# Kernel tuning notes

Hardware: AMD Instinct MI355X
Metric: run time of the kernel (lower is better)

## Reference

```python
import jax, jax.numpy as jnp
import numpy as np

TAU = 0.5  # init tau
EPS = 1e-8  # F.cosine_similarity eps


def setup_inputs() -> dict:
    key = jax.random.key(0)
    k1, k2 = jax.random.split(key)
    N, D, NUM_CLASSES = 4096, 1024, 128
    layer_embeds = jax.random.normal(k1, (N, D), dtype=jnp.float32)
    y_true = jax.random.randint(k2, (N,), 0, NUM_CLASSES, dtype=jnp.int64)
    return {"layer_embeds": layer_embeds, "y_true": y_true}


def reference(layer_embeds, y_true):
    N = layer_embeds.shape[0]
    # batched cosine similarity, scaled like the original: (cos + 1) * 0.5 * tau
    norms = jnp.maximum(jnp.linalg.norm(layer_embeds, axis=1), EPS)  # [N]
    cos = (layer_embeds @ layer_embeds.T) / (norms[:, None] * norms[None, :])  # [N, N]
    S = (cos + 1.0) * 0.5 * TAU

    same = y_true[:, None] == y_true[None, :]  # [N, N]
    eye = jnp.eye(N, dtype=bool)
    pos_mask = same & ~eye            # same-label pairs, j != i
    neg_mask = ~same                  # different-label pairs (diag excluded since same there)

    # column 0: first positive (in j order), else stays 0
    has_pos = pos_mask.any(axis=1)
    first_pos = jnp.argmax(pos_mask, axis=1)
    pos_val = jnp.where(has_pos, S[jnp.arange(N), first_pos], 0.0)  # [N]

    # negatives fill columns 1.. in j order: col = 1 + (#negatives with j' < j)
    negi = neg_mask.astype(jnp.int32)
    col = 1 + jnp.cumsum(negi, axis=1) - negi  # [N, N]
    W = 2 * N  # pad one dummy column for non-negative entries
    cols = jnp.where(neg_mask, col, W - 1)
    rows = jnp.broadcast_to(jnp.arange(N)[:, None], (N, N))
    loss_temp = jnp.zeros((N, W), dtype=jnp.float32)
    loss_temp = loss_temp.at[rows, cols].set(jnp.where(neg_mask, S, 0.0))
    loss_temp = loss_temp.at[:, 0].set(pos_val)
    loss_temp = loss_temp[:, : 2 * N - 1]  # [N, 2N-1], matches torch buffer

    # -log_softmax, take column 0, sum over rows, divide by N
    lse = jax.nn.logsumexp(loss_temp, axis=1)  # [N]
    loss = jnp.sum(lse - loss_temp[:, 0]) / N
    return loss
```

## Files before the change

### kernel.cpp

```cpp
#include <hip/hip_runtime.h>
#include <hip/hip_bf16.h>
#include <math.h>

#define NN 4096
#define DD 1024
#define NCLS 128
#define TAU 0.5f
#define EPSV 1e-8f
#define NB_GEMM 528

typedef __bf16 bf16;
typedef __bf16 bf16x8 __attribute__((ext_vector_type(8)));
typedef __bf16 bf16x4 __attribute__((ext_vector_type(4)));
typedef float f32x4 __attribute__((ext_vector_type(4)));

__device__ __forceinline__ void gl2lds16(const void* g, void* l) {
    __builtin_amdgcn_global_load_lds(
        (const __attribute__((address_space(1))) void*)g,
        (__attribute__((address_space(3))) void*)l,
        16, 0, 0);
}

__global__ __launch_bounds__(256) void k_prep(const float* __restrict__ X,
                                              const int* __restrict__ y,
                                              bf16* __restrict__ Xn,
                                              float* __restrict__ rsum,
                                              float* __restrict__ posv,
                                              int* __restrict__ cnt,
                                              int* __restrict__ fpos) {
    const int t = threadIdx.x;
    if (blockIdx.x == 0) {
        __shared__ int sc[NCLS], s1[NCLS], s2[NCLS];
        if (t < NCLS) { sc[t] = 0; s1[t] = 0x7fffffff; s2[t] = 0x7fffffff; }
        __syncthreads();
        int yv[16];
#pragma unroll
        for (int k = 0; k < 16; ++k) {
            int i = t + k * 256;
            yv[k] = y[i];
            atomicAdd(&sc[yv[k]], 1);
            atomicMin(&s1[yv[k]], i);
        }
        __syncthreads();
#pragma unroll
        for (int k = 0; k < 16; ++k) {
            int i = t + k * 256;
            if (s1[yv[k]] != i) atomicMin(&s2[yv[k]], i);
        }
        __syncthreads();
#pragma unroll
        for (int k = 0; k < 16; ++k) {
            int i = t + k * 256;
            int c = yv[k];
            fpos[i] = (sc[c] >= 2) ? (s1[c] == i ? s2[c] : s1[c]) : -1;
        }
        if (t < NCLS) cnt[t] = sc[t];
        return;
    }
    const int w = t >> 6, lane = t & 63;
    const int row = (blockIdx.x - 1) * 4 + w;
    const float* xr = X + (size_t)row * DD;
    float4 v[4];
    float ss = 0.f;
#pragma unroll
    for (int c = 0; c < 4; ++c) {
        v[c] = *(const float4*)(xr + c * 256 + lane * 4);
        ss += v[c].x * v[c].x + v[c].y * v[c].y + v[c].z * v[c].z + v[c].w * v[c].w;
    }
#pragma unroll
    for (int m = 1; m < 64; m <<= 1) ss += __shfl_xor(ss, m, 64);
    float rn = 1.f / fmaxf(sqrtf(ss), EPSV);
    if (lane == 0) { rsum[row] = 0.f; posv[row] = 0.f; }
#pragma unroll
    for (int c = 0; c < 4; ++c) {
        bf16x4 o;
        o.x = (bf16)(v[c].x * rn);
        o.y = (bf16)(v[c].y * rn);
        o.z = (bf16)(v[c].z * rn);
        o.w = (bf16)(v[c].w * rn);
        *(bf16x4*)(Xn + (size_t)row * DD + c * 256 + lane * 4) = o;
    }
}

__global__ __launch_bounds__(512, 4) void k_gemm(const bf16* __restrict__ Xn,
                                                 const int* __restrict__ y,
                                                 const int* __restrict__ fpos,
                                                 float* __restrict__ rowsum,
                                                 float* __restrict__ posv) {
    __shared__ __align__(16) bf16 As[2][128 * 32];
    __shared__ __align__(16) bf16 Bs[2][128 * 32];
    __shared__ int yA[128], yB[128], fA[128], fB[128];

    int id = (blockIdx.x & 7) * 66 + (blockIdx.x >> 3);
    float ff = sqrtf((float)(8 * id + 1));
    int bj = (int)((ff - 1.f) * 0.5f);
    if (bj * (bj + 1) / 2 > id) bj--;
    if ((bj + 1) * (bj + 2) / 2 <= id) bj++;
    int bi = id - bj * (bj + 1) / 2;
    const int rowA0 = bi * 128;
    const int rowB0 = bj * 128;
    const bool diag = (bi == bj);

    const int tid = threadIdx.x;
    if (tid < 128) { yA[tid] = y[rowA0 + tid]; fA[tid] = fpos[rowA0 + tid]; }
    else if (tid < 256) { yB[tid - 128] = y[rowB0 + tid - 128]; fB[tid - 128] = fpos[rowB0 + tid - 128]; }

    const int lane = tid & 63;
    const int w = tid >> 6;
    const int wm = w & 1, wn = w >> 1;
    const int lr = lane >> 4, lc = lane & 15;

    f32x4 acc[4][2];
#pragma unroll
    for (int i = 0; i < 4; ++i)
#pragma unroll
        for (int j = 0; j < 2; ++j) acc[i][j] = (f32x4){0.f, 0.f, 0.f, 0.f};

    const int r = tid >> 2;
    const int g = tid & 3;
    const int kg = g ^ ((r >> 1) & 3);
    const bf16* gA = Xn + (size_t)(rowA0 + r) * DD + kg * 8;
    const bf16* gB = Xn + (size_t)(rowB0 + r) * DD + kg * 8;
    const int loff = tid * 8;

    const int sw = (lc >> 1) & 3;

    gl2lds16(gA, &As[0][loff]);
    gl2lds16(gB, &Bs[0][loff]);
    __syncthreads();

    int cur = 0;
    for (int k0 = 0; k0 < DD; k0 += 32) {
        if (k0 + 32 < DD) {
            gl2lds16(gA + k0 + 32, &As[cur ^ 1][loff]);
            gl2lds16(gB + k0 + 32, &Bs[cur ^ 1][loff]);
        }
        bf16x8 af[4], bfr[2];
#pragma unroll
        for (int mt = 0; mt < 4; ++mt)
            af[mt] = *(const bf16x8*)(&As[cur][(wm * 64 + mt * 16 + lc) * 32 + ((lr ^ sw) * 8)]);
#pragma unroll
        for (int nt = 0; nt < 2; ++nt)
            bfr[nt] = *(const bf16x8*)(&Bs[cur][(wn * 32 + nt * 16 + lc) * 32 + ((lr ^ sw) * 8)]);
#pragma unroll
        for (int mt = 0; mt < 4; ++mt)
#pragma unroll
            for (int nt = 0; nt < 2; ++nt)
                acc[mt][nt] = __builtin_amdgcn_mfma_f32_16x16x32_bf16(
                    af[mt], bfr[nt], acc[mt][nt], 0, 0, 0);
        __syncthreads();
        cur ^= 1;
    }

    int cloc[2], ycol[2], fcol[2];
    bool pcol[2];
#pragma unroll
    for (int nt = 0; nt < 2; ++nt) {
        cloc[nt] = wn * 32 + nt * 16 + lc;
        ycol[nt] = yB[cloc[nt]];
        fcol[nt] = fB[cloc[nt]];
        pcol[nt] = ((unsigned)(fcol[nt] - rowA0) < 128u);
    }
    float colacc[2] = {0.f, 0.f};
#pragma unroll
    for (int mt = 0; mt < 4; ++mt) {
#pragma unroll
        for (int rr = 0; rr < 4; ++rr) {
            int rloc = wm * 64 + mt * 16 + lr * 4 + rr;
            int rglob = rowA0 + rloc;
            int yrow = yA[rloc];
            int fprow = fA[rloc];
            bool prow = ((unsigned)(fprow - rowB0) < 128u);
            float s = 0.f;
#pragma unroll
            for (int nt = 0; nt < 2; ++nt) {
                float Sv = (acc[mt][nt][rr] + 1.f) * (0.5f * TAU);
                int cg = rowB0 + cloc[nt];
                if (prow && cg == fprow) posv[rglob] = Sv;
                if (pcol[nt] && fcol[nt] == rglob) posv[cg] = Sv;
                float e = (ycol[nt] != yrow) ? __expf(Sv) : 0.f;
                s += e;
                colacc[nt] += e;
            }
            s += __shfl_xor(s, 1, 16);
            s += __shfl_xor(s, 2, 16);
            s += __shfl_xor(s, 4, 16);
            s += __shfl_xor(s, 8, 16);
            if (lc == 0) atomicAdd(&rowsum[rglob], s);
        }
    }
    if (!diag) {
#pragma unroll
        for (int nt = 0; nt < 2; ++nt) {
            float cs = colacc[nt];
            cs += __shfl_xor(cs, 16, 64);
            cs += __shfl_xor(cs, 32, 64);
            if (lane < 16) atomicAdd(&rowsum[rowB0 + wn * 32 + nt * 16 + lane], cs);
        }
    }
}

__global__ __launch_bounds__(1024) void k_finalize(const float* __restrict__ rowsum,
                                                   const float* __restrict__ posv,
                                                   const int* __restrict__ y,
                                                   const int* __restrict__ cnt,
                                                   float* __restrict__ out) {
    int t = threadIdx.x;
    float acc = 0.f;
#pragma unroll
    for (int k = 0; k < 4; ++k) {
        int i = t + k * 1024;
        float pv = posv[i];
        float tot = rowsum[i] + __expf(pv) + (float)(NN - 2 + cnt[y[i]]);
        acc += logf(tot) - pv;
    }
#pragma unroll
    for (int m = 1; m < 64; m <<= 1) acc += __shfl_xor(acc, m, 64);
    __shared__ float wsum[16];
    int w = t >> 6, lane = t & 63;
    if (lane == 0) wsum[w] = acc;
    __syncthreads();
    if (t == 0) {
        float s = 0.f;
#pragma unroll
        for (int q = 0; q < 16; ++q) s += wsum[q];
        *out = s / (float)NN;
    }
}

extern "C" void kernel_launch(void* const* d_in, const int* in_sizes, int n_in,
                              void* d_out, int out_size, void* d_ws, size_t ws_size,
                              hipStream_t stream) {
    const float* X = (const float*)d_in[0];
    const int* y = (const int*)d_in[1];
    float* out = (float*)d_out;

    char* ws = (char*)d_ws;
    bf16* Xn    = (bf16*)ws;
    float* rsum = (float*)(ws + 8 * 1024 * 1024);
    float* posv = (float*)(ws + 8 * 1024 * 1024 + 16 * 1024);
    int* cnt    = (int*)(ws + 8 * 1024 * 1024 + 32 * 1024);
    int* fpos   = (int*)(ws + 8 * 1024 * 1024 + 36 * 1024);

    k_prep<<<dim3(NN / 4 + 1), 256, 0, stream>>>(X, y, Xn, rsum, posv, cnt, fpos);
    k_gemm<<<dim3(NB_GEMM), 512, 0, stream>>>(Xn, y, fpos, rsum, posv);
    k_finalize<<<dim3(1), 1024, 0, stream>>>(rsum, posv, y, cnt, out);
}
```

Measured before the change: 112.7 us.

## Deepen GEMM LDS pipeline to four stages with explicit vmcnt waits

The GEMM main loop moves from a double-buffered LDS scheme to a four-stage ring buffer. Tiles are prefetched three steps ahead, and hand-placed s_waitcnt vmcnt/lgkmcnt waits plus raw barriers replace __syncthreads, so global-to-LDS copies overlap more MFMA work. The last three tiles are peeled into an explicit epilogue. The per-block label and first-positive LDS staging arrays are dropped and read straight from global memory in the epilogue, which offsets part of the extra LDS use. LDS per block doubles, which could limit occupancy, and the epilogue now does more global loads.

```diff
diff --git a/kernel.cpp b/kernel.cpp
--- a/kernel.cpp
+++ b/kernel.cpp
@@ -8,6 +8,7 @@
 #define TAU 0.5f
 #define EPSV 1e-8f
 #define NB_GEMM 528
+#define NT 32
 
 typedef __bf16 bf16;
 typedef __bf16 bf16x8 __attribute__((ext_vector_type(8)));
@@ -87,9 +88,8 @@
                                                  const int* __restrict__ fpos,
                                                  float* __restrict__ rowsum,
                                                  float* __restrict__ posv) {
-    __shared__ __align__(16) bf16 As[2][128 * 32];
-    __shared__ __align__(16) bf16 Bs[2][128 * 32];
-    __shared__ int yA[128], yB[128], fA[128], fB[128];
+    __shared__ __align__(16) bf16 As[4][128 * 32];
+    __shared__ __align__(16) bf16 Bs[4][128 * 32];
 
     int id = (blockIdx.x & 7) * 66 + (blockIdx.x >> 3);
     float ff = sqrtf((float)(8 * id + 1));
@@ -102,9 +102,6 @@
     const bool diag = (bi == bj);
 
     const int tid = threadIdx.x;
-    if (tid < 128) { yA[tid] = y[rowA0 + tid]; fA[tid] = fpos[rowA0 + tid]; }
-    else if (tid < 256) { yB[tid - 128] = y[rowB0 + tid - 128]; fB[tid - 128] = fpos[rowB0 + tid - 128]; }
-
     const int lane = tid & 63;
     const int w = tid >> 6;
     const int wm = w & 1, wn = w >> 1;
@@ -125,40 +122,61 @@
 
     const int sw = (lc >> 1) & 3;
 
-    gl2lds16(gA, &As[0][loff]);
-    gl2lds16(gB, &Bs[0][loff]);
-    __syncthreads();
-
-    int cur = 0;
-    for (int k0 = 0; k0 < DD; k0 += 32) {
-        if (k0 + 32 < DD) {
-            gl2lds16(gA + k0 + 32, &As[cur ^ 1][loff]);
-            gl2lds16(gB + k0 + 32, &Bs[cur ^ 1][loff]);
-        }
+    auto compute = [&](int buf) {
         bf16x8 af[4], bfr[2];
 #pragma unroll
         for (int mt = 0; mt < 4; ++mt)
-            af[mt] = *(const bf16x8*)(&As[cur][(wm * 64 + mt * 16 + lc) * 32 + ((lr ^ sw) * 8)]);
+            af[mt] = *(const bf16x8*)(&As[buf][(wm * 64 + mt * 16 + lc) * 32 + ((lr ^ sw) * 8)]);
 #pragma unroll
         for (int nt = 0; nt < 2; ++nt)
-            bfr[nt] = *(const bf16x8*)(&Bs[cur][(wn * 32 + nt * 16 + lc) * 32 + ((lr ^ sw) * 8)]);
+            bfr[nt] = *(const bf16x8*)(&Bs[buf][(wn * 32 + nt * 16 + lc) * 32 + ((lr ^ sw) * 8)]);
 #pragma unroll
         for (int mt = 0; mt < 4; ++mt)
 #pragma unroll
             for (int nt = 0; nt < 2; ++nt)
                 acc[mt][nt] = __builtin_amdgcn_mfma_f32_16x16x32_bf16(
                     af[mt], bfr[nt], acc[mt][nt], 0, 0, 0);
-        __syncthreads();
-        cur ^= 1;
-    }
+    };
+
+#pragma unroll
+    for (int pt = 0; pt < 4; ++pt) {
+        gl2lds16(gA + pt * 32, &As[pt][loff]);
+        gl2lds16(gB + pt * 32, &Bs[pt][loff]);
+    }
+
+#pragma unroll 4
+    for (int t = 0; t < 29; ++t) {
+        asm volatile("s_waitcnt vmcnt(6)" ::: "memory");
+        __builtin_amdgcn_s_barrier();
+        compute(t & 3);
+        asm volatile("s_waitcnt lgkmcnt(0)" ::: "memory");
+        __builtin_amdgcn_s_barrier();
+        if (t + 4 < NT) {
+            gl2lds16(gA + (t + 4) * 32, &As[t & 3][loff]);
+            gl2lds16(gB + (t + 4) * 32, &Bs[t & 3][loff]);
+        }
+    }
+    asm volatile("s_waitcnt vmcnt(4)" ::: "memory");
+    __builtin_amdgcn_s_barrier();
+    compute(1);
+    asm volatile("s_waitcnt lgkmcnt(0)" ::: "memory");
+    __builtin_amdgcn_s_barrier();
+    asm volatile("s_waitcnt vmcnt(2)" ::: "memory");
+    __builtin_amdgcn_s_barrier();
+    compute(2);
+    asm volatile("s_waitcnt lgkmcnt(0)" ::: "memory");
+    __builtin_amdgcn_s_barrier();
+    asm volatile("s_waitcnt vmcnt(0)" ::: "memory");
+    __builtin_amdgcn_s_barrier();
+    compute(3);
 
     int cloc[2], ycol[2], fcol[2];
     bool pcol[2];
 #pragma unroll
     for (int nt = 0; nt < 2; ++nt) {
         cloc[nt] = wn * 32 + nt * 16 + lc;
-        ycol[nt] = yB[cloc[nt]];
-        fcol[nt] = fB[cloc[nt]];
+        ycol[nt] = y[rowB0 + cloc[nt]];
+        fcol[nt] = fpos[rowB0 + cloc[nt]];
         pcol[nt] = ((unsigned)(fcol[nt] - rowA0) < 128u);
     }
     float colacc[2] = {0.f, 0.f};
@@ -168,8 +186,8 @@
         for (int rr = 0; rr < 4; ++rr) {
             int rloc = wm * 64 + mt * 16 + lr * 4 + rr;
             int rglob = rowA0 + rloc;
-            int yrow = yA[rloc];
-            int fprow = fA[rloc];
+            int yrow = y[rglob];
+            int fprow = fpos[rglob];
             bool prow = ((unsigned)(fprow - rowB0) < 128u);
             float s = 0.f;
 #pragma unroll
```

Result: slower. 122.9 us (+9.0%).

## Switch symmetric GEMM to 128x64 tiles with finer triangular block mapping

Applied to the files above, without the earlier changes.

Replaces the 128x128 upper-triangle tiling with 512-thread blocks by 128x64 tiles with 256 threads. This doubles the block count to 1056 for better load balance across CUs and cuts wasted work on the diagonal. Diagonal tiles are now handled by masking with rglob < cg so every pair is counted once through both row and column sums. The label and first-positive caches in LDS are dropped in favour of direct global loads, which adds redundant global reads in the epilogue. The smaller B tile means less data reuse per block.

```diff
diff --git a/kernel.cpp b/kernel.cpp
--- a/kernel.cpp
+++ b/kernel.cpp
@@ -7,7 +7,7 @@
 #define NCLS 128
 #define TAU 0.5f
 #define EPSV 1e-8f
-#define NB_GEMM 528
+#define NB_GEMM 1056
 
 typedef __bf16 bf16;
 typedef __bf16 bf16x8 __attribute__((ext_vector_type(8)));
@@ -82,29 +82,23 @@
     }
 }
 
-__global__ __launch_bounds__(512, 4) void k_gemm(const bf16* __restrict__ Xn,
-                                                 const int* __restrict__ y,
-                                                 const int* __restrict__ fpos,
-                                                 float* __restrict__ rowsum,
-                                                 float* __restrict__ posv) {
+__global__ __launch_bounds__(256) void k_gemm(const bf16* __restrict__ Xn,
+                                              const int* __restrict__ y,
+                                              const int* __restrict__ fpos,
+                                              float* __restrict__ rowsum,
+                                              float* __restrict__ posv) {
     __shared__ __align__(16) bf16 As[2][128 * 32];
-    __shared__ __align__(16) bf16 Bs[2][128 * 32];
-    __shared__ int yA[128], yB[128], fA[128], fB[128];
-
-    int id = (blockIdx.x & 7) * 66 + (blockIdx.x >> 3);
-    float ff = sqrtf((float)(8 * id + 1));
-    int bj = (int)((ff - 1.f) * 0.5f);
-    if (bj * (bj + 1) / 2 > id) bj--;
-    if ((bj + 1) * (bj + 2) / 2 <= id) bj++;
-    int bi = id - bj * (bj + 1) / 2;
+    __shared__ __align__(16) bf16 Bs[2][64 * 32];
+
+    int id = (blockIdx.x & 7) * 132 + (blockIdx.x >> 3);
+    int bi = (int)((65.f - sqrtf((float)(4225 - 4 * id))) * 0.5f);
+    while (bi * (65 - bi) > id) bi--;
+    while ((bi + 1) * (64 - bi) <= id) bi++;
+    int bj = 2 * bi + (id - bi * (65 - bi));
     const int rowA0 = bi * 128;
-    const int rowB0 = bj * 128;
-    const bool diag = (bi == bj);
+    const int rowB0 = bj * 64;
 
     const int tid = threadIdx.x;
-    if (tid < 128) { yA[tid] = y[rowA0 + tid]; fA[tid] = fpos[rowA0 + tid]; }
-    else if (tid < 256) { yB[tid - 128] = y[rowB0 + tid - 128]; fB[tid - 128] = fpos[rowB0 + tid - 128]; }
-
     const int lane = tid & 63;
     const int w = tid >> 6;
     const int wm = w & 1, wn = w >> 1;
@@ -119,21 +113,24 @@
     const int r = tid >> 2;
     const int g = tid & 3;
     const int kg = g ^ ((r >> 1) & 3);
-    const bf16* gA = Xn + (size_t)(rowA0 + r) * DD + kg * 8;
-    const bf16* gB = Xn + (size_t)(rowB0 + r) * DD + kg * 8;
+    const bf16* gA0 = Xn + (size_t)(rowA0 + r) * DD + kg * 8;
+    const bf16* gA1 = gA0 + (size_t)64 * DD;
+    const bf16* gB  = Xn + (size_t)(rowB0 + r) * DD + kg * 8;
     const int loff = tid * 8;
 
     const int sw = (lc >> 1) & 3;
 
-    gl2lds16(gA, &As[0][loff]);
-    gl2lds16(gB, &Bs[0][loff]);
+    gl2lds16(gA0, &As[0][loff]);
+    gl2lds16(gA1, &As[0][2048 + loff]);
+    gl2lds16(gB,  &Bs[0][loff]);
     __syncthreads();
 
     int cur = 0;
     for (int k0 = 0; k0 < DD; k0 += 32) {
         if (k0 + 32 < DD) {
-            gl2lds16(gA + k0 + 32, &As[cur ^ 1][loff]);
-            gl2lds16(gB + k0 + 32, &Bs[cur ^ 1][loff]);
+            gl2lds16(gA0 + k0 + 32, &As[cur ^ 1][loff]);
+            gl2lds16(gA1 + k0 + 32, &As[cur ^ 1][2048 + loff]);
+            gl2lds16(gB  + k0 + 32, &Bs[cur ^ 1][loff]);
         }
         bf16x8 af[4], bfr[2];
 #pragma unroll
@@ -157,8 +154,8 @@
 #pragma unroll
     for (int nt = 0; nt < 2; ++nt) {
         cloc[nt] = wn * 32 + nt * 16 + lc;
-        ycol[nt] = yB[cloc[nt]];
-        fcol[nt] = fB[cloc[nt]];
+        ycol[nt] = y[rowB0 + cloc[nt]];
+        fcol[nt] = fpos[rowB0 + cloc[nt]];
         pcol[nt] = ((unsigned)(fcol[nt] - rowA0) < 128u);
     }
     float colacc[2] = {0.f, 0.f};
@@ -168,9 +165,9 @@
         for (int rr = 0; rr < 4; ++rr) {
             int rloc = wm * 64 + mt * 16 + lr * 4 + rr;
             int rglob = rowA0 + rloc;
-            int yrow = yA[rloc];
-            int fprow = fA[rloc];
-            bool prow = ((unsigned)(fprow - rowB0) < 128u);
+            int yrow = y[rglob];
+            int fprow = fpos[rglob];
+            bool prow = ((unsigned)(fprow - rowB0) < 64u);
             float s = 0.f;
 #pragma unroll
             for (int nt = 0; nt < 2; ++nt) {
@@ -178,7 +175,7 @@
                 int cg = rowB0 + cloc[nt];
                 if (prow && cg == fprow) posv[rglob] = Sv;
                 if (pcol[nt] && fcol[nt] == rglob) posv[cg] = Sv;
-                float e = (ycol[nt] != yrow) ? __expf(Sv) : 0.f;
+                float e = (ycol[nt] != yrow && rglob < cg) ? __expf(Sv) : 0.f;
                 s += e;
                 colacc[nt] += e;
             }
@@ -189,14 +186,12 @@
             if (lc == 0) atomicAdd(&rowsum[rglob], s);
         }
     }
-    if (!diag) {
-#pragma unroll
-        for (int nt = 0; nt < 2; ++nt) {
-            float cs = colacc[nt];
-            cs += __shfl_xor(cs, 16, 64);
-            cs += __shfl_xor(cs, 32, 64);
-            if (lane < 16) atomicAdd(&rowsum[rowB0 + wn * 32 + nt * 16 + lane], cs);
-        }
+#pragma unroll
+    for (int nt = 0; nt < 2; ++nt) {
+        float cs = colacc[nt];
+        cs += __shfl_xor(cs, 16, 64);
+        cs += __shfl_xor(cs, 32, 64);
+        if (lane < 16) atomicAdd(&rowsum[rowB0 + wn * 32 + nt * 16 + lane], cs);
     }
 }
 
@@ -243,6 +238,6 @@
     int* fpos   = (int*)(ws + 8 * 1024 * 1024 + 36 * 1024);
 
     k_prep<<<dim3(NN / 4 + 1), 256, 0, stream>>>(X, y, Xn, rsum, posv, cnt, fpos);
-    k_gemm<<<dim3(NB_GEMM), 512, 0, stream>>>(Xn, y, fpos, rsum, posv);
+    k_gemm<<<dim3(NB_GEMM), 256, 0, stream>>>(Xn, y, fpos, rsum, posv);
     k_finalize<<<dim3(1), 1024, 0, stream>>>(rsum, posv, y, cnt, out);
 }
```

Measured after the change: 137.0 us. 1.22x slower.
